# Kernel tuning notes

Measured on AMD Instinct MI355X. Metric: run time of the kernel, lower is better.

## Reference

```python
import jax, jax.numpy as jnp
import numpy as np

T, B, D, H = 1024, 256, 128, 128


def setup_inputs() -> dict:
    key = jax.random.key(0)
    k1, k2, k3, k4, k5 = jax.random.split(key, 5)
    seq = jax.random.normal(k1, (T, B, D), dtype=jnp.float32)
    resets = jax.random.bernoulli(k2, p=0.01, shape=(T, B))
    initial_carry = jax.random.normal(k3, (B, H), dtype=jnp.float32)
    # GRU params: input proj (no bias, flax convention) and hidden proj (bias)
    Wi = jax.random.normal(k4, (D, 3 * H), dtype=jnp.float32) / np.sqrt(D)
    Wh = jax.random.normal(k5, (H, 3 * H), dtype=jnp.float32) / np.sqrt(H)
    bh = jnp.zeros((3 * H,), dtype=jnp.float32)
    return {"seq": seq, "resets": resets, "initial_carry": initial_carry,
            "Wi": Wi, "Wh": Wh, "bh": bh}


def _gru_cell(h, x, Wi, Wh, bh):
    # flax GRUCell math: r,z,n gates; input dense has no bias, hidden dense has bias
    gi = x @ Wi                      # [B, 3H]
    gh = h @ Wh + bh                 # [B, 3H]
    i_r, i_z, i_n = jnp.split(gi, 3, axis=-1)
    h_r, h_z, h_n = jnp.split(gh, 3, axis=-1)
    r = jax.nn.sigmoid(i_r + h_r)
    z = jax.nn.sigmoid(i_z + h_z)
    n = jnp.tanh(i_n + r * h_n)
    new_h = (1.0 - z) * n + z * h
    return new_h


def reference(seq, resets, initial_carry, Wi, Wh, bh):
    def step_fn(carry, x):
        inp, reset = x
        # reset-masked carry: where reset, restart from initial_carry
        carry = jnp.where(reset[..., None], initial_carry, carry)
        new_h = _gru_cell(carry, inp, Wi, Wh, bh)
        return new_h, new_h
    final_carry, ys = jax.lax.scan(step_fn, initial_carry, (seq, resets))
    return final_carry, ys
```

## Files before the change

kernel.cpp:

```cpp
#include <hip/hip_runtime.h>
#include <hip/hip_bf16.h>


#define T_STEPS 1024
#define B_SZ 256
#define D_SZ 128
#define H_SZ 128

#define SC_RZ 1.44269504f
#define SC_N  2.88539008f

typedef _Float16 f16x4 __attribute__((ext_vector_type(4)));
typedef _Float16 f16x8 __attribute__((ext_vector_type(8)));
typedef float f32x4 __attribute__((ext_vector_type(4)));

__device__ __forceinline__ float fastrcp(float x) {
#if __has_builtin(__builtin_amdgcn_rcpf)
  return __builtin_amdgcn_rcpf(x);
#else
  return 1.0f / x;
#endif
}

__device__ __forceinline__ float fexp2(float x) {
#if __has_builtin(__builtin_amdgcn_exp2f)
  return __builtin_amdgcn_exp2f(x);
#else
  return __builtin_exp2f(x);
#endif
}

#define BARL() asm volatile("s_waitcnt lgkmcnt(0)\n\ts_barrier" ::: "memory")

#define LOADX(TT_, Y_) { \
    int tl_ = (TT_) + s; if (tl_ > T_STEPS - 1) tl_ = T_STEPS - 1; \
    const float* xp_ = &seq[((size_t)tl_ * B_SZ + b) * D_SZ + q * 8]; \
    Y_[0] = *(const float4*)(xp_ + 0);   Y_[1] = *(const float4*)(xp_ + 4); \
    Y_[2] = *(const float4*)(xp_ + 32);  Y_[3] = *(const float4*)(xp_ + 36); \
    Y_[4] = *(const float4*)(xp_ + 64);  Y_[5] = *(const float4*)(xp_ + 68); \
    Y_[6] = *(const float4*)(xp_ + 96);  Y_[7] = *(const float4*)(xp_ + 100); }

#define PRODUCE(PD_, Y_) { \
    f16x8 xf_[4]; \
    _Pragma("unroll") for (int kk_ = 0; kk_ < 4; kk_++) { \
      f16x8 f_; \
      f_[0] = (_Float16)Y_[2*kk_].x;   f_[1] = (_Float16)Y_[2*kk_].y; \
      f_[2] = (_Float16)Y_[2*kk_].z;   f_[3] = (_Float16)Y_[2*kk_].w; \
      f_[4] = (_Float16)Y_[2*kk_+1].x; f_[5] = (_Float16)Y_[2*kk_+1].y; \
      f_[6] = (_Float16)Y_[2*kk_+1].z; f_[7] = (_Float16)Y_[2*kk_+1].w; \
      xf_[kk_] = f_; } \
    f32x4 ac_[3][2]; \
    _Pragma("unroll") for (int g3_ = 0; g3_ < 3; g3_++) \
      _Pragma("unroll") for (int c2_ = 0; c2_ < 2; c2_++) { \
        const float bv_ = (g3_ == 2) ? 0.f : biasS[g3_][c2_]; \
        ac_[g3_][c2_] = (f32x4){bv_, bv_, bv_, bv_}; } \
    _Pragma("unroll") for (int kk_ = 0; kk_ < 4; kk_++) \
      _Pragma("unroll") for (int g3_ = 0; g3_ < 3; g3_++) \
        _Pragma("unroll") for (int c2_ = 0; c2_ < 2; c2_++) \
          ac_[g3_][c2_] = __builtin_amdgcn_mfma_f32_16x16x32_f16( \
              xf_[kk_], wiF[g3_][c2_][kk_], ac_[g3_][c2_], 0, 0, 0); \
    _Pragma("unroll") for (int c2_ = 0; c2_ < 2; c2_++) \
      _Pragma("unroll") for (int j_ = 0; j_ < 4; j_++) { \
        f16x4 pv_; \
        pv_[0] = (_Float16)ac_[0][c2_][j_]; \
        pv_[1] = (_Float16)ac_[1][c2_][j_]; \
        pv_[2] = (_Float16)ac_[2][c2_][j_]; \
        pv_[3] = (_Float16)0.f; \
        *(f16x4*)&gil[PD_][q * 4 + j_][w * 32 + c2_ * 16 + s][0] = pv_; } }

#define STEPF(T_, G_, RN_, PP_) { \
    const int p_ = (T_) & 1; \
    f16x8 hf0_ = *(const f16x8*)&ht[p_][ 0 + q * 8]; \
    f16x8 hf1_ = *(const f16x8*)&ht[p_][32 + q * 8]; \
    f16x8 hf2_ = *(const f16x8*)&ht[p_][64 + q * 8]; \
    f16x8 hf3_ = *(const f16x8*)&ht[p_][96 + q * 8]; \
    const float gr_ = (float)G_[0], gz_ = (float)G_[1], gn_ = (float)G_[2]; \
    G_ = *(const f16x4*)&gil[PP_][((T_) + 4) & 15][cq][0]; \
    f32x4 aR0_ = __builtin_amdgcn_mfma_f32_16x16x32_f16(hf0_, whF[0][0][0], Z4, 0, 0, 0); \
    f32x4 aR1_ = __builtin_amdgcn_mfma_f32_16x16x32_f16(hf0_, whF[0][1][0], Z4, 0, 0, 0); \
    aR0_ = __builtin_amdgcn_mfma_f32_16x16x32_f16(hf1_, whF[0][0][1], aR0_, 0, 0, 0); \
    aR1_ = __builtin_amdgcn_mfma_f32_16x16x32_f16(hf1_, whF[0][1][1], aR1_, 0, 0, 0); \
    aR0_ = __builtin_amdgcn_mfma_f32_16x16x32_f16(hf2_, whF[0][0][2], aR0_, 0, 0, 0); \
    aR1_ = __builtin_amdgcn_mfma_f32_16x16x32_f16(hf2_, whF[0][1][2], aR1_, 0, 0, 0); \
    aR0_ = __builtin_amdgcn_mfma_f32_16x16x32_f16(hf3_, whF[0][0][3], aR0_, 0, 0, 0); \
    aR1_ = __builtin_amdgcn_mfma_f32_16x16x32_f16(hf3_, whF[0][1][3], aR1_, 0, 0, 0); \
    f32x4 aZ0_ = __builtin_amdgcn_mfma_f32_16x16x32_f16(hf0_, whF[1][0][0], Z4, 0, 0, 0); \
    f32x4 aZ1_ = __builtin_amdgcn_mfma_f32_16x16x32_f16(hf0_, whF[1][1][0], Z4, 0, 0, 0); \
    aZ0_ = __builtin_amdgcn_mfma_f32_16x16x32_f16(hf1_, whF[1][0][1], aZ0_, 0, 0, 0); \
    aZ1_ = __builtin_amdgcn_mfma_f32_16x16x32_f16(hf1_, whF[1][1][1], aZ1_, 0, 0, 0); \
    aZ0_ = __builtin_amdgcn_mfma_f32_16x16x32_f16(hf2_, whF[1][0][2], aZ0_, 0, 0, 0); \
    aZ1_ = __builtin_amdgcn_mfma_f32_16x16x32_f16(hf2_, whF[1][1][2], aZ1_, 0, 0, 0); \
    aZ0_ = __builtin_amdgcn_mfma_f32_16x16x32_f16(hf3_, whF[1][0][3], aZ0_, 0, 0, 0); \
    aZ1_ = __builtin_amdgcn_mfma_f32_16x16x32_f16(hf3_, whF[1][1][3], aZ1_, 0, 0, 0); \
    f32x4 aN0_ = __builtin_amdgcn_mfma_f32_16x16x32_f16(hf0_, whF[2][0][0], Z4, 0, 0, 0); \
    f32x4 aN1_ = __builtin_amdgcn_mfma_f32_16x16x32_f16(hf0_, whF[2][1][0], Z4, 0, 0, 0); \
    aN0_ = __builtin_amdgcn_mfma_f32_16x16x32_f16(hf1_, whF[2][0][1], aN0_, 0, 0, 0); \
    aN1_ = __builtin_amdgcn_mfma_f32_16x16x32_f16(hf1_, whF[2][1][1], aN1_, 0, 0, 0); \
    aN0_ = __builtin_amdgcn_mfma_f32_16x16x32_f16(hf2_, whF[2][0][2], aN0_, 0, 0, 0); \
    aN1_ = __builtin_amdgcn_mfma_f32_16x16x32_f16(hf2_, whF[2][1][2], aN1_, 0, 0, 0); \
    aN0_ = __builtin_amdgcn_mfma_f32_16x16x32_f16(hf3_, whF[2][0][3], aN0_, 0, 0, 0); \
    aN1_ = __builtin_amdgcn_mfma_f32_16x16x32_f16(hf3_, whF[2][1][3], aN1_, 0, 0, 0); \
    const float sR_ = (cg ? aR1_[0] : aR0_[0]) + gr_; \
    const float r_ = fastrcp(1.f + fexp2(-sR_)); \
    const float sZ_ = (cg ? aZ1_[0] : aZ0_[0]) + gz_; \
    const float z_ = fastrcp(1.f + fexp2(-sZ_)); \
    const float sN_ = (cg ? aN1_[0] : aN0_[0]) + bh_n; \
    const float e2_ = fexp2(gn_ + r_ * sN_); \
    const float n_ = 1.f - 2.f * fastrcp(e2_ + 1.f); \
    const float hnew_ = n_ + z_ * (hu - n_); \
    hu = (RN_) ? h0c : hnew_; \
    if (wrH) ht[p_ ^ 1][cq] = (_Float16)hu; \
    else ys[((size_t)(T_) * B_SZ + b) * H_SZ + cq] = hnew_; \
    yfin = hnew_; \
    BARL(); }

__global__ __launch_bounds__(256, 1)
void gru_fused(const float* __restrict__ seq,
               const int* __restrict__ resets,
               const float* __restrict__ h0,
               const float* __restrict__ Wi,
               const float* __restrict__ Wh,
               const float* __restrict__ bh,
               float* __restrict__ out) {
  const int b = blockIdx.x;
  const int tid = threadIdx.x;
  const int w = tid >> 6;
  const int lane = tid & 63;
  const int q = lane >> 4;
  const int s = lane & 15;
  const int cg = q >> 1;
  const int cq = w * 32 + (cg << 4) + s;
  const bool wrH = ((q & 1) == 0);

  __shared__ int rsts[T_STEPS];
  __shared__ __align__(16) _Float16 ht[2][H_SZ];
  __shared__ __align__(16) _Float16 gil[2][16][132][4];

  for (int i = tid; i < T_STEPS; i += 256)
    rsts[i] = (i < T_STEPS - 1) ? resets[(size_t)(i + 1) * B_SZ + b] : 0;

  f16x8 whF[3][2][4], wiF[3][2][4];
  float biasS[2][2];
#pragma unroll
  for (int g3 = 0; g3 < 3; g3++) {
    const float sc = (g3 == 2) ? SC_N : SC_RZ;
#pragma unroll
    for (int c2 = 0; c2 < 2; c2++) {
      const int col = g3 * H_SZ + w * 32 + c2 * 16 + s;
      if (g3 < 2) biasS[g3][c2] = SC_RZ * bh[col];
#pragma unroll
      for (int kk = 0; kk < 4; kk++) {
        f16x8 fh, fi;
#pragma unroll
        for (int e = 0; e < 8; e++) {
          const size_t ko = (size_t)(kk * 32 + q * 8 + e) * 384 + col;
          fh[e] = (_Float16)(sc * Wh[ko]);
          fi[e] = (_Float16)(sc * Wi[ko]);
        }
        whF[g3][c2][kk] = fh;
        wiF[g3][c2][kk] = fi;
      }
    }
  }

  const f32x4 Z4 = {0.f, 0.f, 0.f, 0.f};
  const float bh_n = SC_N * bh[2 * H_SZ + cq];
  const float h0c = h0[(size_t)b * H_SZ + cq];
  float hu = h0c;
  float yfin = h0c;

  if (tid < H_SZ) ht[0][tid] = (_Float16)h0[(size_t)b * H_SZ + tid];

  float4 ya[8];
  LOADX(0, ya)
  PRODUCE(0, ya)
  LOADX(16, ya)
  __syncthreads();

  f16x4 gA = *(const f16x4*)&gil[0][0][cq][0];
  f16x4 gB = *(const f16x4*)&gil[0][1][cq][0];
  f16x4 gC = *(const f16x4*)&gil[0][2][cq][0];
  f16x4 gD = *(const f16x4*)&gil[0][3][cq][0];

  float* ys = out + (size_t)B_SZ * H_SZ;

#pragma unroll 1
  for (int T0 = 0; T0 < T_STEPS; T0 += 16) {
    const int par = (T0 >> 4) & 1;
    const int parx = par ^ 1;
    PRODUCE(parx, ya)
    LOADX(T0 + 32, ya)
    const int4 r0 = *(const int4*)&rsts[T0];
    const int4 r1 = *(const int4*)&rsts[T0 + 4];
    const int4 r2 = *(const int4*)&rsts[T0 + 8];
    const int4 r3 = *(const int4*)&rsts[T0 + 12];
    STEPF(T0 + 0,  gA, r0.x, par)
    STEPF(T0 + 1,  gB, r0.y, par)
    STEPF(T0 + 2,  gC, r0.z, par)
    STEPF(T0 + 3,  gD, r0.w, par)
    STEPF(T0 + 4,  gA, r1.x, par)
    STEPF(T0 + 5,  gB, r1.y, par)
    STEPF(T0 + 6,  gC, r1.z, par)
    STEPF(T0 + 7,  gD, r1.w, par)
    STEPF(T0 + 8,  gA, r2.x, par)
    STEPF(T0 + 9,  gB, r2.y, par)
    STEPF(T0 + 10, gC, r2.z, par)
    STEPF(T0 + 11, gD, r2.w, par)
    STEPF(T0 + 12, gA, r3.x, parx)
    STEPF(T0 + 13, gB, r3.y, parx)
    STEPF(T0 + 14, gC, r3.z, parx)
    STEPF(T0 + 15, gD, r3.w, parx)
  }
  if (wrH) out[(size_t)b * H_SZ + cq] = yfin;
}

extern "C" void kernel_launch(void* const* d_in, const int* in_sizes, int n_in,
                              void* d_out, int out_size, void* d_ws, size_t ws_size,
                              hipStream_t stream) {
  const float* seq    = (const float*)d_in[0];
  const int*   resets = (const int*)d_in[1];
  const float* h0     = (const float*)d_in[2];
  const float* Wi     = (const float*)d_in[3];
  const float* Wh     = (const float*)d_in[4];
  const float* bh     = (const float*)d_in[5];
  (void)in_sizes; (void)n_in; (void)out_size; (void)d_ws; (void)ws_size;

  gru_fused<<<B_SZ, 256, 0, stream>>>(seq, resets, h0, Wi, Wh, bh,
                                      (float*)d_out);
}
```

Measured before the change: 372.6 us.

## Interleave input-projection MFMAs across recurrent steps and reorder gate computation

The input-projection work for the next 16-step chunk used to run as one batch of 24 MFMAs at the start of each chunk. It is now split into pairs, one pair placed inside each of the first 12 recurrent steps. The global load, the f16 store to shared memory and the conversion are spread across steps in the same way. The hidden-state MFMAs are also reordered to R, N, Z, and the z-gate math moves after n, so the r and n dependency chain starts earlier. The aim is to hide the per-chunk projection burst behind the latency-bound serial steps, at the cost of more live registers and extra MFMAs on the critical path of each step.

```diff
diff --git a/kernel.cpp b/kernel.cpp
--- a/kernel.cpp
+++ b/kernel.cpp
@@ -32,43 +32,45 @@
 
 #define BARL() asm volatile("s_waitcnt lgkmcnt(0)\n\ts_barrier" ::: "memory")
 
-#define LOADX(TT_, Y_) { \
+#define LOADX(TT_) { \
     int tl_ = (TT_) + s; if (tl_ > T_STEPS - 1) tl_ = T_STEPS - 1; \
     const float* xp_ = &seq[((size_t)tl_ * B_SZ + b) * D_SZ + q * 8]; \
-    Y_[0] = *(const float4*)(xp_ + 0);   Y_[1] = *(const float4*)(xp_ + 4); \
-    Y_[2] = *(const float4*)(xp_ + 32);  Y_[3] = *(const float4*)(xp_ + 36); \
-    Y_[4] = *(const float4*)(xp_ + 64);  Y_[5] = *(const float4*)(xp_ + 68); \
-    Y_[6] = *(const float4*)(xp_ + 96);  Y_[7] = *(const float4*)(xp_ + 100); }
-
-#define PRODUCE(PD_, Y_) { \
-    f16x8 xf_[4]; \
+    ya[0] = *(const float4*)(xp_ + 0);   ya[1] = *(const float4*)(xp_ + 4); \
+    ya[2] = *(const float4*)(xp_ + 32);  ya[3] = *(const float4*)(xp_ + 36); \
+    ya[4] = *(const float4*)(xp_ + 64);  ya[5] = *(const float4*)(xp_ + 68); \
+    ya[6] = *(const float4*)(xp_ + 96);  ya[7] = *(const float4*)(xp_ + 100); }
+
+#define PCVT() { \
     _Pragma("unroll") for (int kk_ = 0; kk_ < 4; kk_++) { \
       f16x8 f_; \
-      f_[0] = (_Float16)Y_[2*kk_].x;   f_[1] = (_Float16)Y_[2*kk_].y; \
-      f_[2] = (_Float16)Y_[2*kk_].z;   f_[3] = (_Float16)Y_[2*kk_].w; \
-      f_[4] = (_Float16)Y_[2*kk_+1].x; f_[5] = (_Float16)Y_[2*kk_+1].y; \
-      f_[6] = (_Float16)Y_[2*kk_+1].z; f_[7] = (_Float16)Y_[2*kk_+1].w; \
-      xf_[kk_] = f_; } \
-    f32x4 ac_[3][2]; \
+      f_[0] = (_Float16)ya[2*kk_].x;   f_[1] = (_Float16)ya[2*kk_].y; \
+      f_[2] = (_Float16)ya[2*kk_].z;   f_[3] = (_Float16)ya[2*kk_].w; \
+      f_[4] = (_Float16)ya[2*kk_+1].x; f_[5] = (_Float16)ya[2*kk_+1].y; \
+      f_[6] = (_Float16)ya[2*kk_+1].z; f_[7] = (_Float16)ya[2*kk_+1].w; \
+      xf[kk_] = f_; } }
+
+#define PINIT() { \
     _Pragma("unroll") for (int g3_ = 0; g3_ < 3; g3_++) \
-      _Pragma("unroll") for (int c2_ = 0; c2_ < 2; c2_++) { \
-        const float bv_ = (g3_ == 2) ? 0.f : biasS[g3_][c2_]; \
-        ac_[g3_][c2_] = (f32x4){bv_, bv_, bv_, bv_}; } \
-    _Pragma("unroll") for (int kk_ = 0; kk_ < 4; kk_++) \
-      _Pragma("unroll") for (int g3_ = 0; g3_ < 3; g3_++) \
-        _Pragma("unroll") for (int c2_ = 0; c2_ < 2; c2_++) \
-          ac_[g3_][c2_] = __builtin_amdgcn_mfma_f32_16x16x32_f16( \
-              xf_[kk_], wiF[g3_][c2_][kk_], ac_[g3_][c2_], 0, 0, 0); \
+    _Pragma("unroll") for (int c2_ = 0; c2_ < 2; c2_++) { \
+      const float bv_ = (g3_ == 2) ? 0.f : biasS[g3_][c2_]; \
+      acp[g3_][c2_] = (f32x4){bv_, bv_, bv_, bv_}; } }
+
+#define PM(M_) \
+    acp[((M_) % 6) >> 1][(M_) & 1] = __builtin_amdgcn_mfma_f32_16x16x32_f16( \
+        xf[(M_) / 6], wiF[((M_) % 6) >> 1][(M_) & 1][(M_) / 6], \
+        acp[((M_) % 6) >> 1][(M_) & 1], 0, 0, 0);
+
+#define PSTORE(PD_) { \
     _Pragma("unroll") for (int c2_ = 0; c2_ < 2; c2_++) \
-      _Pragma("unroll") for (int j_ = 0; j_ < 4; j_++) { \
-        f16x4 pv_; \
-        pv_[0] = (_Float16)ac_[0][c2_][j_]; \
-        pv_[1] = (_Float16)ac_[1][c2_][j_]; \
-        pv_[2] = (_Float16)ac_[2][c2_][j_]; \
-        pv_[3] = (_Float16)0.f; \
-        *(f16x4*)&gil[PD_][q * 4 + j_][w * 32 + c2_ * 16 + s][0] = pv_; } }
-
-#define STEPF(T_, G_, RN_, PP_) { \
+    _Pragma("unroll") for (int j_ = 0; j_ < 4; j_++) { \
+      f16x4 pv_; \
+      pv_[0] = (_Float16)acp[0][c2_][j_]; \
+      pv_[1] = (_Float16)acp[1][c2_][j_]; \
+      pv_[2] = (_Float16)acp[2][c2_][j_]; \
+      pv_[3] = (_Float16)0.f; \
+      *(f16x4*)&gil[PD_][q * 4 + j_][w * 32 + c2_ * 16 + s][0] = pv_; } }
+
+#define STEPF(T_, G_, RN_, PP_, ...) { \
     const int p_ = (T_) & 1; \
     f16x8 hf0_ = *(const f16x8*)&ht[p_][ 0 + q * 8]; \
     f16x8 hf1_ = *(const f16x8*)&ht[p_][32 + q * 8]; \
@@ -76,6 +78,8 @@
     f16x8 hf3_ = *(const f16x8*)&ht[p_][96 + q * 8]; \
     const float gr_ = (float)G_[0], gz_ = (float)G_[1], gn_ = (float)G_[2]; \
     G_ = *(const f16x4*)&gil[PP_][((T_) + 4) & 15][cq][0]; \
+    __VA_ARGS__ \
+     \
     f32x4 aR0_ = __builtin_amdgcn_mfma_f32_16x16x32_f16(hf0_, whF[0][0][0], Z4, 0, 0, 0); \
     f32x4 aR1_ = __builtin_amdgcn_mfma_f32_16x16x32_f16(hf0_, whF[0][1][0], Z4, 0, 0, 0); \
     aR0_ = __builtin_amdgcn_mfma_f32_16x16x32_f16(hf1_, whF[0][0][1], aR0_, 0, 0, 0); \
@@ -84,6 +88,16 @@
     aR1_ = __builtin_amdgcn_mfma_f32_16x16x32_f16(hf2_, whF[0][1][2], aR1_, 0, 0, 0); \
     aR0_ = __builtin_amdgcn_mfma_f32_16x16x32_f16(hf3_, whF[0][0][3], aR0_, 0, 0, 0); \
     aR1_ = __builtin_amdgcn_mfma_f32_16x16x32_f16(hf3_, whF[0][1][3], aR1_, 0, 0, 0); \
+     \
+    f32x4 aN0_ = __builtin_amdgcn_mfma_f32_16x16x32_f16(hf0_, whF[2][0][0], Z4, 0, 0, 0); \
+    f32x4 aN1_ = __builtin_amdgcn_mfma_f32_16x16x32_f16(hf0_, whF[2][1][0], Z4, 0, 0, 0); \
+    aN0_ = __builtin_amdgcn_mfma_f32_16x16x32_f16(hf1_, whF[2][0][1], aN0_, 0, 0, 0); \
+    aN1_ = __builtin_amdgcn_mfma_f32_16x16x32_f16(hf1_, whF[2][1][1], aN1_, 0, 0, 0); \
+    aN0_ = __builtin_amdgcn_mfma_f32_16x16x32_f16(hf2_, whF[2][0][2], aN0_, 0, 0, 0); \
+    aN1_ = __builtin_amdgcn_mfma_f32_16x16x32_f16(hf2_, whF[2][1][2], aN1_, 0, 0, 0); \
+    aN0_ = __builtin_amdgcn_mfma_f32_16x16x32_f16(hf3_, whF[2][0][3], aN0_, 0, 0, 0); \
+    aN1_ = __builtin_amdgcn_mfma_f32_16x16x32_f16(hf3_, whF[2][1][3], aN1_, 0, 0, 0); \
+     \
     f32x4 aZ0_ = __builtin_amdgcn_mfma_f32_16x16x32_f16(hf0_, whF[1][0][0], Z4, 0, 0, 0); \
     f32x4 aZ1_ = __builtin_amdgcn_mfma_f32_16x16x32_f16(hf0_, whF[1][1][0], Z4, 0, 0, 0); \
     aZ0_ = __builtin_amdgcn_mfma_f32_16x16x32_f16(hf1_, whF[1][0][1], aZ0_, 0, 0, 0); \
@@ -92,21 +106,13 @@
     aZ1_ = __builtin_amdgcn_mfma_f32_16x16x32_f16(hf2_, whF[1][1][2], aZ1_, 0, 0, 0); \
     aZ0_ = __builtin_amdgcn_mfma_f32_16x16x32_f16(hf3_, whF[1][0][3], aZ0_, 0, 0, 0); \
     aZ1_ = __builtin_amdgcn_mfma_f32_16x16x32_f16(hf3_, whF[1][1][3], aZ1_, 0, 0, 0); \
-    f32x4 aN0_ = __builtin_amdgcn_mfma_f32_16x16x32_f16(hf0_, whF[2][0][0], Z4, 0, 0, 0); \
-    f32x4 aN1_ = __builtin_amdgcn_mfma_f32_16x16x32_f16(hf0_, whF[2][1][0], Z4, 0, 0, 0); \
-    aN0_ = __builtin_amdgcn_mfma_f32_16x16x32_f16(hf1_, whF[2][0][1], aN0_, 0, 0, 0); \
-    aN1_ = __builtin_amdgcn_mfma_f32_16x16x32_f16(hf1_, whF[2][1][1], aN1_, 0, 0, 0); \
-    aN0_ = __builtin_amdgcn_mfma_f32_16x16x32_f16(hf2_, whF[2][0][2], aN0_, 0, 0, 0); \
-    aN1_ = __builtin_amdgcn_mfma_f32_16x16x32_f16(hf2_, whF[2][1][2], aN1_, 0, 0, 0); \
-    aN0_ = __builtin_amdgcn_mfma_f32_16x16x32_f16(hf3_, whF[2][0][3], aN0_, 0, 0, 0); \
-    aN1_ = __builtin_amdgcn_mfma_f32_16x16x32_f16(hf3_, whF[2][1][3], aN1_, 0, 0, 0); \
     const float sR_ = (cg ? aR1_[0] : aR0_[0]) + gr_; \
     const float r_ = fastrcp(1.f + fexp2(-sR_)); \
-    const float sZ_ = (cg ? aZ1_[0] : aZ0_[0]) + gz_; \
-    const float z_ = fastrcp(1.f + fexp2(-sZ_)); \
     const float sN_ = (cg ? aN1_[0] : aN0_[0]) + bh_n; \
     const float e2_ = fexp2(gn_ + r_ * sN_); \
     const float n_ = 1.f - 2.f * fastrcp(e2_ + 1.f); \
+    const float sZ_ = (cg ? aZ1_[0] : aZ0_[0]) + gz_; \
+    const float z_ = fastrcp(1.f + fexp2(-sZ_)); \
     const float hnew_ = n_ + z_ * (hu - n_); \
     hu = (RN_) ? h0c : hnew_; \
     if (wrH) ht[p_ ^ 1][cq] = (_Float16)hu; \
@@ -115,13 +121,13 @@
     BARL(); }
 
 __global__ __launch_bounds__(256, 1)
-void gru_fused(const float* __restrict__ seq,
-               const int* __restrict__ resets,
-               const float* __restrict__ h0,
-               const float* __restrict__ Wi,
-               const float* __restrict__ Wh,
-               const float* __restrict__ bh,
-               float* __restrict__ out) {
+void gru_fused2(const float* __restrict__ seq,
+                const int* __restrict__ resets,
+                const float* __restrict__ h0,
+                const float* __restrict__ Wi,
+                const float* __restrict__ Wh,
+                const float* __restrict__ bh,
+                float* __restrict__ out) {
   const int b = blockIdx.x;
   const int tid = threadIdx.x;
   const int w = tid >> 6;
@@ -172,9 +178,19 @@
   if (tid < H_SZ) ht[0][tid] = (_Float16)h0[(size_t)b * H_SZ + tid];
 
   float4 ya[8];
-  LOADX(0, ya)
-  PRODUCE(0, ya)
-  LOADX(16, ya)
+  f16x8 xf[4];
+  f32x4 acp[3][2];
+
+  LOADX(0)
+  PCVT()
+  PINIT()
+  PM(0)  PM(1)  PM(2)  PM(3)  PM(4)  PM(5)  PM(6)  PM(7)
+  PM(8)  PM(9)  PM(10) PM(11) PM(12) PM(13) PM(14) PM(15)
+  PM(16) PM(17) PM(18) PM(19) PM(20) PM(21) PM(22) PM(23)
+  PSTORE(0)
+  LOADX(16)
+  PCVT()
+  PINIT()
   __syncthreads();
 
   f16x4 gA = *(const f16x4*)&gil[0][0][cq][0];
@@ -188,28 +204,26 @@
   for (int T0 = 0; T0 < T_STEPS; T0 += 16) {
     const int par = (T0 >> 4) & 1;
     const int parx = par ^ 1;
-    PRODUCE(parx, ya)
-    LOADX(T0 + 32, ya)
     const int4 r0 = *(const int4*)&rsts[T0];
     const int4 r1 = *(const int4*)&rsts[T0 + 4];
     const int4 r2 = *(const int4*)&rsts[T0 + 8];
     const int4 r3 = *(const int4*)&rsts[T0 + 12];
-    STEPF(T0 + 0,  gA, r0.x, par)
-    STEPF(T0 + 1,  gB, r0.y, par)
-    STEPF(T0 + 2,  gC, r0.z, par)
-    STEPF(T0 + 3,  gD, r0.w, par)
-    STEPF(T0 + 4,  gA, r1.x, par)
-    STEPF(T0 + 5,  gB, r1.y, par)
-    STEPF(T0 + 6,  gC, r1.z, par)
-    STEPF(T0 + 7,  gD, r1.w, par)
-    STEPF(T0 + 8,  gA, r2.x, par)
-    STEPF(T0 + 9,  gB, r2.y, par)
-    STEPF(T0 + 10, gC, r2.z, par)
-    STEPF(T0 + 11, gD, r2.w, par)
-    STEPF(T0 + 12, gA, r3.x, parx)
-    STEPF(T0 + 13, gB, r3.y, parx)
-    STEPF(T0 + 14, gC, r3.z, parx)
-    STEPF(T0 + 15, gD, r3.w, parx)
+    STEPF(T0 + 0,  gA, r0.x, par,  PM(0)  PM(1))
+    STEPF(T0 + 1,  gB, r0.y, par,  PM(2)  PM(3)  LOADX(T0 + 32))
+    STEPF(T0 + 2,  gC, r0.z, par,  PM(4)  PM(5))
+    STEPF(T0 + 3,  gD, r0.w, par,  PM(6)  PM(7))
+    STEPF(T0 + 4,  gA, r1.x, par,  PM(8)  PM(9))
+    STEPF(T0 + 5,  gB, r1.y, par,  PM(10) PM(11))
+    STEPF(T0 + 6,  gC, r1.z, par,  PM(12) PM(13))
+    STEPF(T0 + 7,  gD, r1.w, par,  PM(14) PM(15))
+    STEPF(T0 + 8,  gA, r2.x, par,  PM(16) PM(17))
+    STEPF(T0 + 9,  gB, r2.y, par,  PM(18) PM(19))
+    STEPF(T0 + 10, gC, r2.z, par,  PM(20) PM(21))
+    STEPF(T0 + 11, gD, r2.w, par,  PM(22) PM(23) PSTORE(parx))
+    STEPF(T0 + 12, gA, r3.x, parx, ;)
+    STEPF(T0 + 13, gB, r3.y, parx, ;)
+    STEPF(T0 + 14, gC, r3.z, parx, ;)
+    STEPF(T0 + 15, gD, r3.w, parx, PCVT() PINIT())
   }
   if (wrH) out[(size_t)b * H_SZ + cq] = yfin;
 }
@@ -225,6 +239,6 @@
   const float* bh     = (const float*)d_in[5];
   (void)in_sizes; (void)n_in; (void)out_size; (void)d_ws; (void)ws_size;
 
-  gru_fused<<<B_SZ, 256, 0, stream>>>(seq, resets, h0, Wi, Wh, bh,
-                                      (float*)d_out);
-}
+  gru_fused2<<<B_SZ, 256, 0, stream>>>(seq, resets, h0, Wi, Wh, bh,
+                                       (float*)d_out);
+}
```

Measured after the change: 378.1 us. No clear change (+1.5%).
